# Performance work log

Hardware: AMD Instinct MI355X
Metric: run time of the kernel (lower is better)

Reference implementation:

```python
import jax, jax.numpy as jnp
import numpy as np
import math

B, W, D, H, K = 32, 512, 512, 8, 64
DH = D // H

def _rms(x, s, eps=1e-6):
    return x / jnp.sqrt(jnp.mean(x * x, axis=-1, keepdims=True) + eps) * s

def _l2n(x):
    return x / (jnp.linalg.norm(x, axis=-1, keepdims=True) + 1e-6)

def _rope(x, fc):
    b, t, h, d = x.shape
    xc = jax.lax.complex(x[..., 0::2], x[..., 1::2])
    xr = xc * fc
    return jnp.stack([xr.real, xr.imag], axis=-1).reshape(b, t, h, d)

def setup_inputs() -> dict:
    key = jax.random.key(0)
    ks = jax.random.split(key, 24)
    n = lambda i, s: jax.random.normal(ks[i], s, jnp.float32) * 0.02
    return {
        'x': jax.random.normal(ks[0], (B, W, D), jnp.float32),
        'epi_keys': _l2n(jax.random.normal(ks[1], (B, K, D), jnp.float32)),
        'epi_vals': jax.random.normal(ks[2], (B, K, D), jnp.float32),
        'epi_age': jax.random.uniform(ks[3], (B, K), jnp.float32, 0.0, 10.0),
        'epi_strength': jax.random.uniform(ks[4], (B, K), jnp.float32, 0.01, 1.0),
        'pos_idx': jnp.arange(W, dtype=jnp.int32),
        'rms1': jnp.ones((D,), jnp.float32), 'rms_kv': jnp.ones((D,), jnp.float32),
        'rms2': jnp.ones((D,), jnp.float32), 'rms_read': jnp.ones((D,), jnp.float32),
        'Wq': n(5, (D, D)), 'bq': jnp.zeros((D,), jnp.float32),
        'Wk': n(6, (D, D)), 'bk': jnp.zeros((D,), jnp.float32),
        'Wv': n(7, (D, D)), 'bv': jnp.zeros((D,), jnp.float32),
        'Wo': n(8, (D, D)), 'bo': jnp.zeros((D,), jnp.float32),
        'W1': n(9, (D, 8 * D)), 'W2': n(10, (4 * D, D)),
        'Wwk': n(11, (D, D)), 'bwk': jnp.zeros((D,), jnp.float32),
        'Wwv': n(12, (D, D)), 'bwv': jnp.zeros((D,), jnp.float32),
        'Wws': n(13, (D, 1)), 'bws': jnp.zeros((1,), jnp.float32),
        'Wg1': n(14, (D + 2, D)), 'bg1': jnp.zeros((D,), jnp.float32),
        'Wg2': n(15, (D, 1)), 'bg2': jnp.zeros((1,), jnp.float32),
    }

def _cell(x, epi_keys, epi_vals, epi_age, epi_strength, pos_idx,
          rms1, rms_kv, rms2, rms_read, Wq, bq, Wk, bk, Wv, bv, Wo, bo,
          W1, W2, Wwk, bwk, Wwv, bwv, Wws, bws, Wg1, bg1, Wg2, bg2):
    Bc, T, Dc = x.shape
    # RoPE freqs at absolute window positions (slice_freqs_cis)
    freqs = 1.0 / (10000.0 ** (jnp.arange(0, DH, 2, dtype=jnp.float32) / DH))  # (DH/2,)
    ang = pos_idx.astype(jnp.float32)[:, None] * freqs[None, :]               # (T, DH/2)
    fc = jax.lax.complex(jnp.cos(ang), jnp.sin(ang))[None, :, None, :]        # (1,T,1,DH/2)
    # --- windowed causal RoPE attention (TransformerBlock) ---
    nx, nkv = _rms(x, rms1), _rms(x, rms_kv)
    q = _rope((nx @ Wq + bq).reshape(Bc, T, H, DH), fc)
    k = _rope((nkv @ Wk + bk).reshape(Bc, T, H, DH), fc)
    v = (nkv @ Wv + bv).reshape(Bc, T, H, DH)
    att = jnp.einsum('bthd,bshd->bhts', q, k) / math.sqrt(DH)
    causal = jnp.tril(jnp.ones((T, T), bool))
    att = jnp.where(causal[None, None], att, -1e9)
    p = jax.nn.softmax(att, axis=-1)
    o = jnp.einsum('bhts,bshd->bthd', p, v).reshape(Bc, T, Dc)
    h1 = x + (o @ Wo + bo)
    gv = _rms(h1, rms2) @ W1
    g, val = jnp.split(gv, 2, axis=-1)
    h2 = h1 + (jax.nn.silu(g) * val) @ W2                                     # (B,T,D)
    # --- window summary query ---
    q_win = jnp.mean(h2, axis=1)                                              # (B,D)
    # --- EpisodicSlotReader ---
    qn = _l2n(q_win)
    kn = _l2n(epi_keys)
    sim_r = jnp.sum(kn * qn[:, None, :], axis=-1)                             # (B,K)
    logits = sim_r + 0.5 * jnp.log(jnp.clip(epi_strength, 0.001, 1e9)) - 0.02 * epi_age
    logits = logits + ((epi_strength > 0.001).astype(jnp.float32) - 1.0) * 1000.0
    w_read = jax.nn.softmax(logits, axis=-1)
    read = _rms(jnp.sum(w_read[:, :, None] * epi_vals, axis=1), rms_read)     # (B,D)
    # --- write projections ---
    write_key = q_win @ Wwk + bwk
    write_val = q_win @ Wwv + bwv
    ws = jnp.clip(jax.nn.sigmoid(q_win @ Wws + bws), 0.0, 1.0)                # (B,1)
    # --- EpisodicSlotWriter (ST top-1 competitive write) ---
    wk_n = _l2n(write_key)
    sim_w = jnp.sum(kn * wk_n[:, None, :], axis=-1)                           # (B,K)
    soft = jax.nn.softmax(sim_w * 50.0, axis=-1)
    hard = jax.nn.one_hot(jnp.argmax(soft, axis=-1), K, dtype=jnp.float32)
    write_w = jax.lax.stop_gradient(hard - soft) + soft
    eff = write_w * ws * 0.5                                                  # (B,K)
    re = eff[:, :, None]
    keys_new = _l2n((1.0 - re) * epi_keys + re * write_key[:, None, :])
    vals_new = (1.0 - re) * epi_vals + re * write_val[:, None, :]
    age_new = (epi_age + 1.0) * (1.0 - write_w)
    sn = epi_strength * 0.995
    sn = jnp.clip(sn + write_w * ws * (1.0 - sn), 0.001, 1.0)
    best_sim = jnp.max(sim_w, axis=-1)                                        # (B,)
    # --- MemoryRecallGate ---
    novelty = (1.0 - best_sim)[:, None]
    xg = jnp.concatenate([q_win, ws, novelty], axis=-1)                       # (B,D+2)
    gate = jax.nn.sigmoid(jax.nn.silu(xg @ Wg1 + bg1) @ Wg2 + bg2)            # (B,1)
    out = h2 + (gate * read)[:, None, :]
    return out, keys_new, vals_new, age_new, sn, gate

def reference(x, epi_keys, epi_vals, epi_age, epi_strength, pos_idx,
              rms1, rms_kv, rms2, rms_read, Wq, bq, Wk, bk, Wv, bv, Wo, bo,
              W1, W2, Wwk, bwk, Wwv, bwv, Wws, bws, Wg1, bg1, Wg2, bg2):
    return _cell(x, epi_keys, epi_vals, epi_age, epi_strength, pos_idx,
                 rms1, rms_kv, rms2, rms_read, Wq, bq, Wk, bk, Wv, bv, Wo, bo,
                 W1, W2, Wwk, bwk, Wwv, bwv, Wws, bws, Wg1, bg1, Wg2, bg2)
```

## Files before the change

### kernel.cpp

```cpp
#include <hip/hip_runtime.h>


#define DEVI __device__ __forceinline__
typedef unsigned short u16;
typedef unsigned int   u32;
typedef __bf16 v8bf __attribute__((ext_vector_type(8)));
typedef float  v4f  __attribute__((ext_vector_type(4)));

DEVI float bf2f(u16 u) { u32 v = ((u32)u) << 16; return __builtin_bit_cast(float, v); }
DEVI u16 f2bf(float f) {
  u32 x = __builtin_bit_cast(u32, f);
  u32 r = x + 0x7fffu + ((x >> 16) & 1u);
  return (u16)(r >> 16);
}
DEVI uint4 pack8(const float* f) {
  u32 a[4];
#pragma unroll
  for (int i = 0; i < 4; ++i)
    a[i] = (u32)f2bf(f[2*i]) | ((u32)f2bf(f[2*i+1]) << 16);
  uint4 v; v.x = a[0]; v.y = a[1]; v.z = a[2]; v.w = a[3]; return v;
}
DEVI void ld8f(const float* p, float* f) {
  float4 a = *(const float4*)p, b = *(const float4*)(p + 4);
  f[0]=a.x; f[1]=a.y; f[2]=a.z; f[3]=a.w; f[4]=b.x; f[5]=b.y; f[6]=b.z; f[7]=b.w;
}
DEVI void st8f(float* p, const float* f) {
  *(float4*)p       = make_float4(f[0], f[1], f[2], f[3]);
  *(float4*)(p + 4) = make_float4(f[4], f[5], f[6], f[7]);
}
DEVI v8bf ldfrag(const u16* p) { return __builtin_bit_cast(v8bf, *(const uint4*)p); }

DEVI void async16(const u16* g, u16* l) {
  __builtin_amdgcn_global_load_lds(
      (const __attribute__((address_space(1))) void*)g,
      (__attribute__((address_space(3))) void*)l, 16, 0, 0);
}

DEVI float wave_sum64(float v) {
  v += __shfl_xor(v, 1);  v += __shfl_xor(v, 2);  v += __shfl_xor(v, 4);
  v += __shfl_xor(v, 8);  v += __shfl_xor(v, 16); v += __shfl_xor(v, 32);
  return v;
}

__device__ float block_sum256(float v, float* sred) {
  v = wave_sum64(v);
  int w = threadIdx.x >> 6;
  __syncthreads();
  if ((threadIdx.x & 63) == 0) sred[w] = v;
  __syncthreads();
  return sred[0] + sred[1] + sred[2] + sred[3];
}

__global__ __launch_bounds__(256) void transpose_k(const float* __restrict__ in,
                                                   const float* __restrict__ scale,
                                                   u16* __restrict__ outp,
                                                   int R, int C) {
  __shared__ u16 t[32][33];
  int c0 = blockIdx.x * 32, r0 = blockIdx.y * 32;
  int lc = threadIdx.x & 31, lr = threadIdx.x >> 5;
  for (int rr = lr; rr < 32; rr += 8) {
    float v = in[(size_t)(r0 + rr) * C + c0 + lc];
    if (scale) v *= scale[r0 + rr];
    t[rr][lc] = f2bf(v);
  }
  __syncthreads();
  for (int rr = lr; rr < 32; rr += 8)
    outp[(size_t)(c0 + rr) * R + r0 + lc] = t[lc][rr];
}

__global__ __launch_bounds__(256) void rms_k(const float* __restrict__ x,
                                             u16* __restrict__ o1) {
  int w = threadIdx.x >> 6, lane = threadIdx.x & 63;
  size_t row = (size_t)blockIdx.x * 4 + w;
  float xf[8]; ld8f(x + row * 512 + lane * 8, xf);
  float ss = 0.f;
#pragma unroll
  for (int i = 0; i < 8; ++i) ss += xf[i] * xf[i];
  ss = wave_sum64(ss);
  float inv = rsqrtf(ss * (1.f / 512.f) + 1e-6f);
  float of[8];
#pragma unroll
  for (int i = 0; i < 8; ++i) of[i] = xf[i] * inv;
  *(uint4*)(o1 + row * 512 + lane * 8) = pack8(of);
}

__global__ __launch_bounds__(256) void gemm128_k(const u16* __restrict__ A,
                                                 const u16* __restrict__ BT,
                                                 const float* __restrict__ bias,
                                                 const float* __restrict__ bias2,
                                                 const float* __restrict__ resf,
                                                 u16* __restrict__ outb,
                                                 float* __restrict__ outf,
                                                 int N, int Kd) {
  __shared__ u16 As[128 * 64];
  __shared__ u16 Bs[128 * 64];
  int tid = threadIdx.x;
  int w = tid >> 6, lane = tid & 63;
  int m = lane & 15, quad = lane >> 4;
  int wm = w >> 1, wn = w & 1;
  int bm = blockIdx.x, bn = blockIdx.y;
  v4f acc[4][4] = {};
  const int gswz = ((lane & 7) ^ (lane >> 3)) * 8;
  const u16* Ag = A + (size_t)(bm * 128 + w * 32 + (lane >> 3)) * Kd + gswz;
  const u16* Bg = BT + (size_t)(bn * 128 + w * 32 + (lane >> 3)) * Kd + gswz;
  u16* Al = &As[w * 32 * 64];
  u16* Bl = &Bs[w * 32 * 64];
  const int rsw = (m & 7) * 8;
  for (int k0 = 0; k0 < Kd; k0 += 64) {
#pragma unroll
    for (int it = 0; it < 4; ++it) {
      async16(Ag + (size_t)it * 8 * Kd + k0, Al + it * 8 * 64);
      async16(Bg + (size_t)it * 8 * Kd + k0, Bl + it * 8 * 64);
    }
    __syncthreads();
#pragma unroll
    for (int kk = 0; kk < 2; ++kk) {
      v8bf af[4], bfr[4];
#pragma unroll
      for (int i = 0; i < 4; ++i)
        af[i] = ldfrag(&As[(wm * 64 + i * 16 + m) * 64 +
                           ((kk * 32 + quad * 8) ^ rsw)]);
#pragma unroll
      for (int j = 0; j < 4; ++j)
        bfr[j] = ldfrag(&Bs[(wn * 64 + j * 16 + m) * 64 +
                            ((kk * 32 + quad * 8) ^ rsw)]);
#pragma unroll
      for (int i = 0; i < 4; ++i)
#pragma unroll
        for (int j = 0; j < 4; ++j)
          acc[i][j] = __builtin_amdgcn_mfma_f32_16x16x32_bf16(af[i], bfr[j],
                                                              acc[i][j], 0, 0, 0);
    }
    __syncthreads();
  }
#pragma unroll
  for (int i = 0; i < 4; ++i) {
    int grow0 = bm * 128 + wm * 64 + i * 16 + quad * 4;
#pragma unroll
    for (int j = 0; j < 4; ++j) {
      int gcol = bn * 128 + wn * 64 + j * 16 + m;
      float bv = 0.f;
      if (bias) {
        int cc = gcol;
        const float* bp = bias;
        if (bias2 && cc >= 512) { bp = bias2; cc -= 512; }
        bv = bp[cc];
      }
#pragma unroll
      for (int rr = 0; rr < 4; ++rr) {
        size_t idx = (size_t)(grow0 + rr) * N + gcol;
        float v = acc[i][j][rr] + bv;
        if (resf) v += resf[idx];
        if (outb) outb[idx] = f2bf(v);
        else      outf[idx] = v;
      }
    }
  }
}

__global__ __launch_bounds__(256) void mlp1_k(const u16* __restrict__ A,
                                              const u16* __restrict__ W1T,
                                              u16* __restrict__ out) {
  __shared__ u16 As[128 * 64];
  __shared__ u16 Bgs[64 * 64];
  __shared__ u16 Bvs[64 * 64];
  const int Kd = 512;
  int tid = threadIdx.x;
  int w = tid >> 6, lane = tid & 63;
  int m = lane & 15, quad = lane >> 4;
  int bm = blockIdx.x, bn = blockIdx.y;
  v4f accg[2][4] = {}, accv[2][4] = {};
  const int gswz = ((lane & 7) ^ (lane >> 3)) * 8;
  const u16* Ag  = A + (size_t)(bm * 128 + w * 32 + (lane >> 3)) * Kd + gswz;
  const u16* Bgp = W1T + (size_t)(bn * 64 + w * 16 + (lane >> 3)) * Kd + gswz;
  const u16* Bvp = W1T + (size_t)(2048 + bn * 64 + w * 16 + (lane >> 3)) * Kd + gswz;
  u16* Al  = &As[w * 32 * 64];
  u16* Bgl = &Bgs[w * 16 * 64];
  u16* Bvl = &Bvs[w * 16 * 64];
  const int rsw = (m & 7) * 8;
  for (int k0 = 0; k0 < Kd; k0 += 64) {
#pragma unroll
    for (int it = 0; it < 4; ++it)
      async16(Ag + (size_t)it * 8 * Kd + k0, Al + it * 8 * 64);
#pragma unroll
    for (int it = 0; it < 2; ++it) {
      async16(Bgp + (size_t)it * 8 * Kd + k0, Bgl + it * 8 * 64);
      async16(Bvp + (size_t)it * 8 * Kd + k0, Bvl + it * 8 * 64);
    }
    __syncthreads();
#pragma unroll
    for (int kk = 0; kk < 2; ++kk) {
      v8bf af[2], bg[4], bv[4];
#pragma unroll
      for (int i = 0; i < 2; ++i)
        af[i] = ldfrag(&As[(w * 32 + i * 16 + m) * 64 +
                           ((kk * 32 + quad * 8) ^ rsw)]);
#pragma unroll
      for (int j = 0; j < 4; ++j) {
        bg[j] = ldfrag(&Bgs[(j * 16 + m) * 64 + ((kk * 32 + quad * 8) ^ rsw)]);
        bv[j] = ldfrag(&Bvs[(j * 16 + m) * 64 + ((kk * 32 + quad * 8) ^ rsw)]);
      }
#pragma unroll
      for (int i = 0; i < 2; ++i)
#pragma unroll
        for (int j = 0; j < 4; ++j) {
          accg[i][j] = __builtin_amdgcn_mfma_f32_16x16x32_bf16(af[i], bg[j],
                                                               accg[i][j], 0, 0, 0);
          accv[i][j] = __builtin_amdgcn_mfma_f32_16x16x32_bf16(af[i], bv[j],
                                                               accv[i][j], 0, 0, 0);
        }
    }
    __syncthreads();
  }
#pragma unroll
  for (int i = 0; i < 2; ++i) {
    int grow0 = bm * 128 + w * 32 + i * 16 + quad * 4;
#pragma unroll
    for (int j = 0; j < 4; ++j) {
      int gcol = bn * 64 + j * 16 + m;
#pragma unroll
      for (int rr = 0; rr < 4; ++rr) {
        float g = accg[i][j][rr];
        float sv = g / (1.f + __expf(-g));
        out[(size_t)(grow0 + rr) * 2048 + gcol] = f2bf(sv * accv[i][j][rr]);
      }
    }
  }
}

__global__ __launch_bounds__(256) void rope_k(u16* __restrict__ tnsr,
                                              const int* __restrict__ pos,
                                              int rowStride) {
  int pid = blockIdx.x * 256 + threadIdx.x;
  int f = pid & 31;
  int row = pid >> 8;
  int tt = row & 511;
  int col2 = (pid & 255) * 2;
  float freq = exp2f(-0.41524101186f * (float)f);
  float ang = (float)pos[tt] * freq;
  float sv, cv;
  sincosf(ang, &sv, &cv);
  u16* p = tnsr + (size_t)row * rowStride + col2;
  u32 v = *(u32*)p;
  float e = bf2f((u16)(v & 0xffffu)), o = bf2f((u16)(v >> 16));
  float ne = e * cv - o * sv;
  float no = e * sv + o * cv;
  *(u32*)p = (u32)f2bf(ne) | ((u32)f2bf(no) << 16);
}

__global__ __launch_bounds__(1024) void attn_k(const u16* __restrict__ qg,
                                               const u16* __restrict__ kv,
                                               u16* __restrict__ og) {
  __shared__ u16 Ks[512 * 64];
  __shared__ u16 Vt[64 * 512];
  __shared__ u16 Ps[16][16 * 40];
  int tid = threadIdx.x;
  int w = tid >> 6, lane = tid & 63;
  int m = lane & 15, quad = lane >> 4;
  int bh = blockIdx.x;
  int b = bh >> 3, h = bh & 7;
  const size_t qbase = (size_t)b * 512 * 512 + h * 64;
  const u16* kbase = kv + (size_t)b * 512 * 1024 + h * 64;
  const u16* vbase = kbase + 512;

  {
    int d8 = (tid & 7) * 8;
    for (int s = tid >> 3; s < 512; s += 128) {
      uint4 t4 = *(const uint4*)(kbase + (size_t)s * 1024 + d8);
      *(uint4*)&Ks[s * 64 + (d8 ^ ((s & 7) * 8))] = t4;
    }
  }
  {
    int d = tid & 63, sw = (d & 7) * 8;
    for (int s = tid >> 6; s < 512; s += 16)
      Vt[d * 512 + (s ^ sw)] = vbase[(size_t)s * 1024 + d];
  }
  __syncthreads();

  for (int rep = 0; rep < 2; ++rep) {
    int qt = rep == 0 ? w : 31 - w;
    int tb = qt * 16;
    const u16* qp = qg + qbase + (size_t)(tb + m) * 512;
    v8bf aq0 = ldfrag(qp + quad * 8);
    v8bf aq1 = ldfrag(qp + 32 + quad * 8);
    v4f acc[4] = {};
    float mr[4], lr_[4];
#pragma unroll
    for (int rr = 0; rr < 4; ++rr) { mr[rr] = -1.0e30f; lr_[rr] = 0.f; }
    int swz = (m & 7) * 8;

    for (int st2 = 0; st2 <= qt; st2 += 2) {
      int srA = st2 * 16 + m;
      v8bf ka0 = ldfrag(&Ks[srA * 64 + ((quad * 8) ^ swz)]);
      v8bf ka1 = ldfrag(&Ks[srA * 64 + ((32 + quad * 8) ^ swz)]);
      v4f s4a = {};
      s4a = __builtin_amdgcn_mfma_f32_16x16x32_bf16(aq0, ka0, s4a, 0, 0, 0);
      s4a = __builtin_amdgcn_mfma_f32_16x16x32_bf16(aq1, ka1, s4a, 0, 0, 0);
      bool haveB = (st2 + 1 <= qt);
      v4f s4b = {};
      if (haveB) {
        int srB = srA + 16;
        v8bf kb0 = ldfrag(&Ks[srB * 64 + ((quad * 8) ^ swz)]);
        v8bf kb1 = ldfrag(&Ks[srB * 64 + ((32 + quad * 8) ^ swz)]);
        s4b = __builtin_amdgcn_mfma_f32_16x16x32_bf16(aq0, kb0, s4b, 0, 0, 0);
        s4b = __builtin_amdgcn_mfma_f32_16x16x32_bf16(aq1, kb1, s4b, 0, 0, 0);
      }
      float sca[4], scb[4];
#pragma unroll
      for (int rr = 0; rr < 4; ++rr) {
        int rowt = tb + quad * 4 + rr;
        sca[rr] = s4a[rr] * 0.125f;
        if (st2 == qt && st2 * 16 + m > rowt) sca[rr] = -1.0e9f;
        scb[rr] = haveB ? s4b[rr] * 0.125f : -1.0e30f;
        if (haveB && st2 + 1 == qt && (st2 + 1) * 16 + m > rowt) scb[rr] = -1.0e9f;
      }
      float pva[4], pvb[4], alpha[4];
#pragma unroll
      for (int rr = 0; rr < 4; ++rr) {
        float v = fmaxf(sca[rr], scb[rr]);
        v = fmaxf(v, __shfl_xor(v, 1));
        v = fmaxf(v, __shfl_xor(v, 2));
        v = fmaxf(v, __shfl_xor(v, 4));
        v = fmaxf(v, __shfl_xor(v, 8));
        float mn = fmaxf(mr[rr], v);
        alpha[rr] = __expf(mr[rr] - mn);
        pva[rr] = __expf(sca[rr] - mn);
        pvb[rr] = __expf(scb[rr] - mn);
        mr[rr] = mn;
      }
#pragma unroll
      for (int rr = 0; rr < 4; ++rr) {
        float s = pva[rr] + pvb[rr];
        s += __shfl_xor(s, 1); s += __shfl_xor(s, 2);
        s += __shfl_xor(s, 4); s += __shfl_xor(s, 8);
        lr_[rr] = lr_[rr] * alpha[rr] + s;
#pragma unroll
        for (int c = 0; c < 4; ++c) acc[c][rr] *= alpha[rr];
        Ps[w][(quad * 4 + rr) * 40 + m]      = f2bf(pva[rr]);
        Ps[w][(quad * 4 + rr) * 40 + 16 + m] = f2bf(pvb[rr]);
      }
      __asm__ volatile("" ::: "memory");
      v8bf pf = ldfrag(&Ps[w][m * 40 + quad * 8]);
#pragma unroll
      for (int c = 0; c < 4; ++c) {
        int drow = c * 16 + m;
        v8bf vf = ldfrag(&Vt[drow * 512 +
                             ((st2 * 16 + quad * 8) ^ ((drow & 7) * 8))]);
        acc[c] = __builtin_amdgcn_mfma_f32_16x16x32_bf16(pf, vf, acc[c], 0, 0, 0);
      }
    }
#pragma unroll
    for (int rr = 0; rr < 4; ++rr) {
      int t = tb + quad * 4 + rr;
      float inv = 1.f / lr_[rr];
      u16* op = og + qbase + (size_t)t * 512;
#pragma unroll
      for (int c = 0; c < 4; ++c) op[c * 16 + m] = f2bf(acc[c][rr] * inv);
    }
  }
}

__global__ __launch_bounds__(256) void qwin_k(const float* __restrict__ h2,
                                              float* __restrict__ part) {
  int bc = blockIdx.x;
  int b = bc >> 3;
  int c = bc & 7;
  int d2 = threadIdx.x * 2;
  float a0 = 0.f, a1 = 0.f;
  for (int i = 0; i < 64; ++i) {
    int t = c * 64 + i;
    float2 v = *(const float2*)(h2 + ((size_t)(b * 512 + t)) * 512 + d2);
    a0 += v.x;
    a1 += v.y;
  }
  part[(size_t)bc * 512 + d2]     = a0;
  part[(size_t)bc * 512 + d2 + 1] = a1;
}

__global__ __launch_bounds__(256) void qw_k(const float* __restrict__ part,
                                            float* __restrict__ qw_g) {
  int b = blockIdx.x;
#pragma unroll
  for (int u = 0; u < 2; ++u) {
    int d = threadIdx.x + u * 256;
    float s = 0.f;
#pragma unroll
    for (int c = 0; c < 8; ++c) s += part[((size_t)b * 8 + c) * 512 + d];
    qw_g[(size_t)b * 512 + d] = s * (1.f / 512.f);
  }
}

__global__ __launch_bounds__(256) void gemv_k(
    const float* __restrict__ qw_g, const float* __restrict__ Wwk,
    const float* __restrict__ bwk, const float* __restrict__ Wwv,
    const float* __restrict__ bwv, const float* __restrict__ Wg1,
    const float* __restrict__ bg1, const float* __restrict__ Wws,
    const float* __restrict__ bws, float* __restrict__ wkey_g,
    float* __restrict__ wval_g, float* __restrict__ abase_g,
    float* __restrict__ ws_g) {
  __shared__ float qs[512];
  __shared__ float prt[4][64];
  __shared__ float sred[8];
  int tid = threadIdx.x;
  int b = blockIdx.y, cg = blockIdx.x;
  qs[tid]       = qw_g[(size_t)b * 512 + tid];
  qs[tid + 256] = qw_g[(size_t)b * 512 + tid + 256];
  __syncthreads();
  if (cg == 24) {
    float p = qs[tid] * Wws[tid] + qs[tid + 256] * Wws[tid + 256];
    float tot = block_sum256(p, sred);
    if (tid == 0) {
      float wsv = 1.f / (1.f + __expf(-(tot + bws[0])));
      ws_g[b] = fminf(fmaxf(wsv, 0.f), 1.f);
    }
    return;
  }
  int sel = cg >> 3;
  int c0 = (cg & 7) * 64;
  const float* W = sel == 0 ? Wwk : (sel == 1 ? Wwv : Wg1);
  const float* bias = sel == 0 ? bwk : (sel == 1 ? bwv : bg1);
  float* dst = sel == 0 ? wkey_g : (sel == 1 ? wval_g : abase_g);
  int kg = tid >> 6, cl = tid & 63;
  const float* Wp = W + (size_t)(kg * 128) * 512 + c0 + cl;
  float acc = 0.f;
#pragma unroll 8
  for (int i = 0; i < 128; ++i) acc += qs[kg * 128 + i] * Wp[(size_t)i * 512];
  prt[kg][cl] = acc;
  __syncthreads();
  if (tid < 64)
    dst[(size_t)b * 512 + c0 + tid] =
        prt[0][tid] + prt[1][tid] + prt[2][tid] + prt[3][tid] + bias[c0 + tid];
}

__global__ __launch_bounds__(256) void epi2_k(
    const float* __restrict__ qw_g, const float* __restrict__ wkey_g,
    const float* __restrict__ wval_g, const float* __restrict__ abase_g,
    const float* __restrict__ ws_g, const float* __restrict__ keys,
    const float* __restrict__ vals, const float* __restrict__ age,
    const float* __restrict__ strength, const float* __restrict__ Wg1,
    const float* __restrict__ Wg2, const float* __restrict__ bg2,
    const float* __restrict__ rms_read, float* __restrict__ read_f,
    float* __restrict__ gate_f, float* __restrict__ keys_out,
    float* __restrict__ vals_out, float* __restrict__ age_out,
    float* __restrict__ sn_out, float* __restrict__ gate_out) {
  int b = blockIdx.x;
  int tid = threadIdx.x;
  int w = tid >> 6, lane = tid & 63;
  __shared__ float qs[512], wkl[512], wvl[512];
  __shared__ float knorm[64], sr[64], swv[64], wread[64];
  __shared__ float sred[8];
  __shared__ float scal[2];
  __shared__ int bestk;
  __shared__ float novs;

  qs[tid]        = qw_g[(size_t)b * 512 + tid];
  qs[tid + 256]  = qw_g[(size_t)b * 512 + tid + 256];
  wkl[tid]       = wkey_g[(size_t)b * 512 + tid];
  wkl[tid + 256] = wkey_g[(size_t)b * 512 + tid + 256];
  wvl[tid]       = wval_g[(size_t)b * 512 + tid];
  wvl[tid + 256] = wval_g[(size_t)b * 512 + tid + 256];
  __syncthreads();
  float ws_s = ws_g[b];
  float p = qs[tid] * qs[tid] + qs[tid + 256] * qs[tid + 256];
  float tot = block_sum256(p, sred);
  if (tid == 0) scal[0] = 1.f / (sqrtf(tot) + 1e-6f);
  p = wkl[tid] * wkl[tid] + wkl[tid + 256] * wkl[tid + 256];
  tot = block_sum256(p, sred);
  if (tid == 0) scal[1] = 1.f / (sqrtf(tot) + 1e-6f);
  __syncthreads();
  float qscale = scal[0], wscale = scal[1];
  for (int k = w; k < 64; k += 4) {
    float kf[8];
    ld8f(keys + ((size_t)b * 64 + k) * 512 + lane * 8, kf);
    float s2 = 0.f, sq = 0.f, sw = 0.f;
#pragma unroll
    for (int i = 0; i < 8; ++i) {
      s2 += kf[i] * kf[i];
      sq += kf[i] * qs[lane * 8 + i];
      sw += kf[i] * wkl[lane * 8 + i];
    }
    s2 = wave_sum64(s2);
    sq = wave_sum64(sq);
    sw = wave_sum64(sw);
    if (lane == 0) {
      float kn = sqrtf(s2) + 1e-6f;
      knorm[k] = kn;
      float st = strength[b * 64 + k];
      float ag = age[b * 64 + k];
      sr[k] = (sq * qscale) / kn + 0.5f * logf(fminf(fmaxf(st, 0.001f), 1e9f)) -
              0.02f * ag + ((st > 0.001f) ? 0.f : -1000.f);
      swv[k] = (sw * wscale) / kn;
    }
  }
  __syncthreads();
  if (w == 0) {
    float v = sr[lane];
    float mx = v;
    mx = fmaxf(mx, __shfl_xor(mx, 1));  mx = fmaxf(mx, __shfl_xor(mx, 2));
    mx = fmaxf(mx, __shfl_xor(mx, 4));  mx = fmaxf(mx, __shfl_xor(mx, 8));
    mx = fmaxf(mx, __shfl_xor(mx, 16)); mx = fmaxf(mx, __shfl_xor(mx, 32));
    float e = __expf(v - mx);
    float sm = wave_sum64(e);
    wread[lane] = e / sm;
  } else if (w == 1) {
    float v = swv[lane];
    int idx = lane;
#pragma unroll
    for (int mm = 1; mm < 64; mm <<= 1) {
      float ov = __shfl_xor(v, mm);
      int oi = __shfl_xor(idx, mm);
      if (ov > v || (ov == v && oi < idx)) { v = ov; idx = oi; }
    }
    if (lane == 0) { bestk = idx; novs = 1.f - v; }
  }
  __syncthreads();
  float rv0 = 0.f, rv1 = 0.f;
  for (int k = 0; k < 64; ++k) {
    float wr = wread[k];
    const float* vp = vals + ((size_t)b * 64 + k) * 512;
    rv0 += wr * vp[tid];
    rv1 += wr * vp[tid + 256];
  }
  p = rv0 * rv0 + rv1 * rv1;
  tot = block_sum256(p, sred);
  float rinv = rsqrtf(tot * (1.f / 512.f) + 1e-6f);
  read_f[(size_t)b * 512 + tid]       = rv0 * rinv * rms_read[tid];
  read_f[(size_t)b * 512 + tid + 256] = rv1 * rinv * rms_read[tid + 256];
  if (tid < 64) {
    int k = tid;
    float hard = (k == bestk) ? 1.f : 0.f;
    float ag = age[b * 64 + k];
    age_out[b * 64 + k] = (ag + 1.f) * (1.f - hard);
    float st = strength[b * 64 + k];
    float s0 = st * 0.995f;
    float snv = s0 + hard * ws_s * (1.f - s0);
    sn_out[b * 64 + k] = fminf(fmaxf(snv, 0.001f), 1.f);
  }
  for (int k = w; k < 64; k += 4) {
    float re = (k == bestk) ? ws_s * 0.5f : 0.f;
    float kf[8], vf[8];
    ld8f(keys + ((size_t)b * 64 + k) * 512 + lane * 8, kf);
    ld8f(vals + ((size_t)b * 64 + k) * 512 + lane * 8, vf);
    float u[8], ss = 0.f;
#pragma unroll
    for (int i = 0; i < 8; ++i) {
      u[i] = (1.f - re) * kf[i] + re * wkl[lane * 8 + i];
      ss += u[i] * u[i];
    }
    ss = wave_sum64(ss);
    float uinv = 1.f / (sqrtf(ss) + 1e-6f);
    float ko[8], vo[8];
#pragma unroll
    for (int i = 0; i < 8; ++i) {
      ko[i] = u[i] * uinv;
      vo[i] = (1.f - re) * vf[i] + re * wvl[lane * 8 + i];
    }
    st8f(keys_out + ((size_t)b * 64 + k) * 512 + lane * 8, ko);
    st8f(vals_out + ((size_t)b * 64 + k) * 512 + lane * 8, vo);
  }
  __syncthreads();
  float nov = novs;
  float a0 = abase_g[(size_t)b * 512 + tid] +
             ws_s * Wg1[(size_t)512 * 512 + tid] +
             nov * Wg1[(size_t)513 * 512 + tid];
  float a1 = abase_g[(size_t)b * 512 + tid + 256] +
             ws_s * Wg1[(size_t)512 * 512 + tid + 256] +
             nov * Wg1[(size_t)513 * 512 + tid + 256];
  float h0 = a0 / (1.f + __expf(-a0));
  float h1v = a1 / (1.f + __expf(-a1));
  float gp = h0 * Wg2[tid] + h1v * Wg2[tid + 256];
  tot = block_sum256(gp, sred);
  if (tid == 0) {
    float g = 1.f / (1.f + __expf(-(tot + bg2[0])));
    gate_f[b] = g;
    gate_out[b] = g;
  }
}

__global__ __launch_bounds__(256) void final_k(const float* __restrict__ h2,
                                               const float* __restrict__ read_f,
                                               const float* __restrict__ gate_f,
                                               float* __restrict__ outp) {
  size_t i2 = ((size_t)blockIdx.x * 256 + threadIdx.x) * 2;
  int b = (int)(i2 >> 18);
  int d = (int)(i2 & 511);
  float g = gate_f[b];
  float2 h = *(const float2*)(h2 + i2);
  outp[i2]     = h.x + g * read_f[b * 512 + d];
  outp[i2 + 1] = h.y + g * read_f[b * 512 + d + 1];
}

extern "C" void kernel_launch(void* const* d_in, const int* in_sizes, int n_in,
                              void* d_out, int out_size, void* d_ws,
                              size_t ws_size, hipStream_t stream) {
  const float* x        = (const float*)d_in[0];
  const float* epi_keys = (const float*)d_in[1];
  const float* epi_vals = (const float*)d_in[2];
  const float* epi_age  = (const float*)d_in[3];
  const float* epi_str  = (const float*)d_in[4];
  const int*   pos      = (const int*)d_in[5];
  const float* rms1     = (const float*)d_in[6];
  const float* rms_kv   = (const float*)d_in[7];
  const float* rms2     = (const float*)d_in[8];
  const float* rms_read = (const float*)d_in[9];
  const float* Wq = (const float*)d_in[10]; const float* bq = (const float*)d_in[11];
  const float* Wk = (const float*)d_in[12]; const float* bk = (const float*)d_in[13];
  const float* Wv = (const float*)d_in[14]; const float* bv = (const float*)d_in[15];
  const float* Wo = (const float*)d_in[16]; const float* bo = (const float*)d_in[17];
  const float* W1 = (const float*)d_in[18]; const float* W2 = (const float*)d_in[19];
  const float* Wwk = (const float*)d_in[20]; const float* bwk = (const float*)d_in[21];
  const float* Wwv = (const float*)d_in[22]; const float* bwv = (const float*)d_in[23];
  const float* Wws = (const float*)d_in[24]; const float* bws = (const float*)d_in[25];
  const float* Wg1 = (const float*)d_in[26]; const float* bg1 = (const float*)d_in[27];
  const float* Wg2 = (const float*)d_in[28]; const float* bg2 = (const float*)d_in[29];

  float* out      = (float*)d_out;
  float* out_main = out;
  float* out_keys = out + 8388608;
  float* out_vals = out + 9437184;
  float* out_age  = out + 10485760;
  float* out_sn   = out + 10487808;
  float* out_gate = out + 10489856;

  char* w8 = (char*)d_ws;
  size_t off = 0;
  auto alloc = [&](size_t bytes) {
    char* pp = w8 + off;
    off += (bytes + 255) & ~(size_t)255;
    return pp;
  };
  u16* WTq  = (u16*)alloc(512 * 512 * 2);
  u16* WTkv = (u16*)alloc((size_t)1024 * 512 * 2);
  u16* WTo  = (u16*)alloc(512 * 512 * 2);
  u16* WT1  = (u16*)alloc((size_t)4096 * 512 * 2);
  u16* WT2  = (u16*)alloc((size_t)512 * 2048 * 2);
  const size_t TB = (size_t)16384 * 512 * 2;
  u16* nrm = (u16*)alloc(TB);
  u16* qb  = (u16*)alloc(TB);
  u16* kvb = (u16*)alloc(2 * TB);
  u16* ob  = (u16*)alloc(TB);
  u16* n2  = (u16*)alloc(TB);
  float* h1f = (float*)alloc((size_t)16384 * 512 * 4);
  u16*   gact = nrm;
  float* h2f  = (float*)ob;
  float* part    = (float*)alloc((size_t)32 * 8 * 512 * 4);
  float* qw_g    = (float*)alloc((size_t)32 * 512 * 4);
  float* wkey_g  = (float*)alloc((size_t)32 * 512 * 4);
  float* wval_g  = (float*)alloc((size_t)32 * 512 * 4);
  float* abase_g = (float*)alloc((size_t)32 * 512 * 4);
  float* ws_g    = (float*)alloc(64 * 4);
  float* read_f  = (float*)alloc((size_t)32 * 512 * 4);
  float* gate_f  = (float*)alloc(64 * 4);

  transpose_k<<<dim3(16, 16), 256, 0, stream>>>(Wq, rms1, WTq, 512, 512);
  transpose_k<<<dim3(16, 16), 256, 0, stream>>>(Wk, rms_kv, WTkv, 512, 512);
  transpose_k<<<dim3(16, 16), 256, 0, stream>>>(Wv, rms_kv, WTkv + 512 * 512, 512, 512);
  transpose_k<<<dim3(16, 16), 256, 0, stream>>>(Wo, nullptr, WTo, 512, 512);
  transpose_k<<<dim3(128, 16), 256, 0, stream>>>(W1, rms2, WT1, 512, 4096);
  transpose_k<<<dim3(16, 64), 256, 0, stream>>>(W2, nullptr, WT2, 2048, 512);
  rms_k<<<4096, 256, 0, stream>>>(x, nrm);
  gemm128_k<<<dim3(128, 4), 256, 0, stream>>>(nrm, WTq, bq, nullptr, nullptr,
                                              qb, nullptr, 512, 512);
  gemm128_k<<<dim3(128, 8), 256, 0, stream>>>(nrm, WTkv, bk, bv, nullptr,
                                              kvb, nullptr, 1024, 512);
  rope_k<<<16384, 256, 0, stream>>>(qb, pos, 512);
  rope_k<<<16384, 256, 0, stream>>>(kvb, pos, 1024);
  attn_k<<<256, 1024, 0, stream>>>(qb, kvb, ob);
  gemm128_k<<<dim3(128, 4), 256, 0, stream>>>(ob, WTo, bo, nullptr, x,
                                              nullptr, h1f, 512, 512);
  rms_k<<<4096, 256, 0, stream>>>(h1f, n2);
  mlp1_k<<<dim3(128, 32), 256, 0, stream>>>(n2, WT1, gact);
  gemm128_k<<<dim3(128, 4), 256, 0, stream>>>(gact, WT2, nullptr, nullptr, h1f,
                                              nullptr, h2f, 512, 2048);
  qwin_k<<<256, 256, 0, stream>>>(h2f, part);
  qw_k<<<32, 256, 0, stream>>>(part, qw_g);
  gemv_k<<<dim3(25, 32), 256, 0, stream>>>(qw_g, Wwk, bwk, Wwv, bwv, Wg1, bg1,
                                           Wws, bws, wkey_g, wval_g, abase_g, ws_g);
  epi2_k<<<32, 256, 0, stream>>>(qw_g, wkey_g, wval_g, abase_g, ws_g, epi_keys,
                                 epi_vals, epi_age, epi_str, Wg1, Wg2, bg2,
                                 rms_read, read_f, gate_f, out_keys, out_vals,
                                 out_age, out_sn, out_gate);
  final_k<<<16384, 256, 0, stream>>>(h2f, read_f, gate_f, out_main);
}
```

Measured before the change: 542.1 us.

## Overlap next K-tile global loads with MFMA compute in GEMM kernels

Measured after the change: 547.1 us. About the same (+0.9%).

```diff
diff --git a/kernel.cpp b/kernel.cpp
--- a/kernel.cpp
+++ b/kernel.cpp
@@ -106,31 +106,44 @@
   u16* Al = &As[w * 32 * 64];
   u16* Bl = &Bs[w * 32 * 64];
   const int rsw = (m & 7) * 8;
-  for (int k0 = 0; k0 < Kd; k0 += 64) {
-#pragma unroll
-    for (int it = 0; it < 4; ++it) {
-      async16(Ag + (size_t)it * 8 * Kd + k0, Al + it * 8 * 64);
-      async16(Bg + (size_t)it * 8 * Kd + k0, Bl + it * 8 * 64);
+  const int nt = Kd >> 6;
+#pragma unroll
+  for (int it = 0; it < 4; ++it) {
+    async16(Ag + (size_t)it * 8 * Kd, Al + it * 8 * 64);
+    async16(Bg + (size_t)it * 8 * Kd, Bl + it * 8 * 64);
+  }
+  __syncthreads();
+  for (int t = 0; t < nt; ++t) {
+    v8bf af[2][4], bfr[2][4];
+#pragma unroll
+    for (int kk = 0; kk < 2; ++kk) {
+#pragma unroll
+      for (int i = 0; i < 4; ++i)
+        af[kk][i] = ldfrag(&As[(wm * 64 + i * 16 + m) * 64 +
+                               ((kk * 32 + quad * 8) ^ rsw)]);
+#pragma unroll
+      for (int j = 0; j < 4; ++j)
+        bfr[kk][j] = ldfrag(&Bs[(wn * 64 + j * 16 + m) * 64 +
+                                ((kk * 32 + quad * 8) ^ rsw)]);
     }
     __syncthreads();
-#pragma unroll
-    for (int kk = 0; kk < 2; ++kk) {
-      v8bf af[4], bfr[4];
+    if (t + 1 < nt) {
+      int k0 = (t + 1) * 64;
+#pragma unroll
+      for (int it = 0; it < 4; ++it) {
+        async16(Ag + (size_t)it * 8 * Kd + k0, Al + it * 8 * 64);
+        async16(Bg + (size_t)it * 8 * Kd + k0, Bl + it * 8 * 64);
+      }
+    }
+#pragma unroll
+    for (int kk = 0; kk < 2; ++kk)
 #pragma unroll
       for (int i = 0; i < 4; ++i)
-        af[i] = ldfrag(&As[(wm * 64 + i * 16 + m) * 64 +
-                           ((kk * 32 + quad * 8) ^ rsw)]);
-#pragma unroll
-      for (int j = 0; j < 4; ++j)
-        bfr[j] = ldfrag(&Bs[(wn * 64 + j * 16 + m) * 64 +
-                            ((kk * 32 + quad * 8) ^ rsw)]);
-#pragma unroll
-      for (int i = 0; i < 4; ++i)
 #pragma unroll
         for (int j = 0; j < 4; ++j)
-          acc[i][j] = __builtin_amdgcn_mfma_f32_16x16x32_bf16(af[i], bfr[j],
+          acc[i][j] = __builtin_amdgcn_mfma_f32_16x16x32_bf16(af[kk][i],
+                                                              bfr[kk][j],
                                                               acc[i][j], 0, 0, 0);
-    }
     __syncthreads();
   }
 #pragma unroll
@@ -178,38 +191,55 @@
   u16* Bgl = &Bgs[w * 16 * 64];
   u16* Bvl = &Bvs[w * 16 * 64];
   const int rsw = (m & 7) * 8;
-  for (int k0 = 0; k0 < Kd; k0 += 64) {
-#pragma unroll
-    for (int it = 0; it < 4; ++it)
-      async16(Ag + (size_t)it * 8 * Kd + k0, Al + it * 8 * 64);
-#pragma unroll
-    for (int it = 0; it < 2; ++it) {
-      async16(Bgp + (size_t)it * 8 * Kd + k0, Bgl + it * 8 * 64);
-      async16(Bvp + (size_t)it * 8 * Kd + k0, Bvl + it * 8 * 64);
+  const int nt = Kd >> 6;
+#pragma unroll
+  for (int it = 0; it < 4; ++it)
+    async16(Ag + (size_t)it * 8 * Kd, Al + it * 8 * 64);
+#pragma unroll
+  for (int it = 0; it < 2; ++it) {
+    async16(Bgp + (size_t)it * 8 * Kd, Bgl + it * 8 * 64);
+    async16(Bvp + (size_t)it * 8 * Kd, Bvl + it * 8 * 64);
+  }
+  __syncthreads();
+  for (int t = 0; t < nt; ++t) {
+    v8bf af[2][2], bg[2][4], bv[2][4];
+#pragma unroll
+    for (int kk = 0; kk < 2; ++kk) {
+#pragma unroll
+      for (int i = 0; i < 2; ++i)
+        af[kk][i] = ldfrag(&As[(w * 32 + i * 16 + m) * 64 +
+                               ((kk * 32 + quad * 8) ^ rsw)]);
+#pragma unroll
+      for (int j = 0; j < 4; ++j) {
+        bg[kk][j] = ldfrag(&Bgs[(j * 16 + m) * 64 + ((kk * 32 + quad * 8) ^ rsw)]);
+        bv[kk][j] = ldfrag(&Bvs[(j * 16 + m) * 64 + ((kk * 32 + quad * 8) ^ rsw)]);
+      }
     }
     __syncthreads();
-#pragma unroll
-    for (int kk = 0; kk < 2; ++kk) {
-      v8bf af[2], bg[4], bv[4];
+    if (t + 1 < nt) {
+      int k0 = (t + 1) * 64;
+#pragma unroll
+      for (int it = 0; it < 4; ++it)
+        async16(Ag + (size_t)it * 8 * Kd + k0, Al + it * 8 * 64);
+#pragma unroll
+      for (int it = 0; it < 2; ++it) {
+        async16(Bgp + (size_t)it * 8 * Kd + k0, Bgl + it * 8 * 64);
+        async16(Bvp + (size_t)it * 8 * Kd + k0, Bvl + it * 8 * 64);
+      }
+    }
+#pragma unroll
+    for (int kk = 0; kk < 2; ++kk)
 #pragma unroll
       for (int i = 0; i < 2; ++i)
-        af[i] = ldfrag(&As[(w * 32 + i * 16 + m) * 64 +
-                           ((kk * 32 + quad * 8) ^ rsw)]);
-#pragma unroll
-      for (int j = 0; j < 4; ++j) {
-        bg[j] = ldfrag(&Bgs[(j * 16 + m) * 64 + ((kk * 32 + quad * 8) ^ rsw)]);
-        bv[j] = ldfrag(&Bvs[(j * 16 + m) * 64 + ((kk * 32 + quad * 8) ^ rsw)]);
-      }
-#pragma unroll
-      for (int i = 0; i < 2; ++i)
 #pragma unroll
         for (int j = 0; j < 4; ++j) {
-          accg[i][j] = __builtin_amdgcn_mfma_f32_16x16x32_bf16(af[i], bg[j],
+          accg[i][j] = __builtin_amdgcn_mfma_f32_16x16x32_bf16(af[kk][i],
+                                                               bg[kk][j],
                                                                accg[i][j], 0, 0, 0);
-          accv[i][j] = __builtin_amdgcn_mfma_f32_16x16x32_bf16(af[i], bv[j],
+          accv[i][j] = __builtin_amdgcn_mfma_f32_16x16x32_bf16(af[kk][i],
+                                                               bv[kk][j],
                                                                accv[i][j], 0, 0, 0);
         }
-    }
     __syncthreads();
   }
 #pragma unroll
```

## Double-buffer shared-memory tiles in GEMM and MLP1 kernels to overlap loads

Applied to the files above, without the earlier changes.

New measurement: 562.2 us. 3.7% more time.

```diff
diff --git a/kernel.cpp b/kernel.cpp
--- a/kernel.cpp
+++ b/kernel.cpp
@@ -92,8 +92,8 @@
                                                  u16* __restrict__ outb,
                                                  float* __restrict__ outf,
                                                  int N, int Kd) {
-  __shared__ u16 As[128 * 64];
-  __shared__ u16 Bs[128 * 64];
+  __shared__ u16 As[2][128 * 64];
+  __shared__ u16 Bs[2][128 * 64];
   int tid = threadIdx.x;
   int w = tid >> 6, lane = tid & 63;
   int m = lane & 15, quad = lane >> 4;
@@ -103,27 +103,29 @@
   const int gswz = ((lane & 7) ^ (lane >> 3)) * 8;
   const u16* Ag = A + (size_t)(bm * 128 + w * 32 + (lane >> 3)) * Kd + gswz;
   const u16* Bg = BT + (size_t)(bn * 128 + w * 32 + (lane >> 3)) * Kd + gswz;
-  u16* Al = &As[w * 32 * 64];
-  u16* Bl = &Bs[w * 32 * 64];
+  const int lw = w * 32 * 64;
   const int rsw = (m & 7) * 8;
-  for (int k0 = 0; k0 < Kd; k0 += 64) {
+  const int nt = Kd >> 6;
+
+  auto stage = [&](int k0, int bi) {
 #pragma unroll
     for (int it = 0; it < 4; ++it) {
-      async16(Ag + (size_t)it * 8 * Kd + k0, Al + it * 8 * 64);
-      async16(Bg + (size_t)it * 8 * Kd + k0, Bl + it * 8 * 64);
-    }
-    __syncthreads();
+      async16(Ag + (size_t)it * 8 * Kd + k0, &As[bi][lw + it * 8 * 64]);
+      async16(Bg + (size_t)it * 8 * Kd + k0, &Bs[bi][lw + it * 8 * 64]);
+    }
+  };
+  auto compute = [&](int bi) {
 #pragma unroll
     for (int kk = 0; kk < 2; ++kk) {
       v8bf af[4], bfr[4];
 #pragma unroll
       for (int i = 0; i < 4; ++i)
-        af[i] = ldfrag(&As[(wm * 64 + i * 16 + m) * 64 +
-                           ((kk * 32 + quad * 8) ^ rsw)]);
+        af[i] = ldfrag(&As[bi][(wm * 64 + i * 16 + m) * 64 +
+                               ((kk * 32 + quad * 8) ^ rsw)]);
 #pragma unroll
       for (int j = 0; j < 4; ++j)
-        bfr[j] = ldfrag(&Bs[(wn * 64 + j * 16 + m) * 64 +
-                            ((kk * 32 + quad * 8) ^ rsw)]);
+        bfr[j] = ldfrag(&Bs[bi][(wn * 64 + j * 16 + m) * 64 +
+                                ((kk * 32 + quad * 8) ^ rsw)]);
 #pragma unroll
       for (int i = 0; i < 4; ++i)
 #pragma unroll
@@ -131,6 +133,16 @@
           acc[i][j] = __builtin_amdgcn_mfma_f32_16x16x32_bf16(af[i], bfr[j],
                                                               acc[i][j], 0, 0, 0);
     }
+  };
+
+  stage(0, 0);
+  __syncthreads();
+  for (int t = 0; t < nt; t += 2) {
+    stage((t + 1) * 64, 1);
+    compute(0);
+    __syncthreads();
+    if (t + 2 < nt) stage((t + 2) * 64, 0);
+    compute(1);
     __syncthreads();
   }
 #pragma unroll
@@ -161,9 +173,9 @@
 __global__ __launch_bounds__(256) void mlp1_k(const u16* __restrict__ A,
                                               const u16* __restrict__ W1T,
                                               u16* __restrict__ out) {
-  __shared__ u16 As[128 * 64];
-  __shared__ u16 Bgs[64 * 64];
-  __shared__ u16 Bvs[64 * 64];
+  __shared__ u16 As[2][128 * 64];
+  __shared__ u16 Bgs[2][64 * 64];
+  __shared__ u16 Bvs[2][64 * 64];
   const int Kd = 512;
   int tid = threadIdx.x;
   int w = tid >> 6, lane = tid & 63;
@@ -174,31 +186,33 @@
   const u16* Ag  = A + (size_t)(bm * 128 + w * 32 + (lane >> 3)) * Kd + gswz;
   const u16* Bgp = W1T + (size_t)(bn * 64 + w * 16 + (lane >> 3)) * Kd + gswz;
   const u16* Bvp = W1T + (size_t)(2048 + bn * 64 + w * 16 + (lane >> 3)) * Kd + gswz;
-  u16* Al  = &As[w * 32 * 64];
-  u16* Bgl = &Bgs[w * 16 * 64];
-  u16* Bvl = &Bvs[w * 16 * 64];
+  const int lwA = w * 32 * 64;
+  const int lwB = w * 16 * 64;
   const int rsw = (m & 7) * 8;
-  for (int k0 = 0; k0 < Kd; k0 += 64) {
+  const int nt = Kd >> 6;
+
+  auto stage = [&](int k0, int bi) {
 #pragma unroll
     for (int it = 0; it < 4; ++it)
-      async16(Ag + (size_t)it * 8 * Kd + k0, Al + it * 8 * 64);
+      async16(Ag + (size_t)it * 8 * Kd + k0, &As[bi][lwA + it * 8 * 64]);
 #pragma unroll
     for (int it = 0; it < 2; ++it) {
-      async16(Bgp + (size_t)it * 8 * Kd + k0, Bgl + it * 8 * 64);
-      async16(Bvp + (size_t)it * 8 * Kd + k0, Bvl + it * 8 * 64);
-    }
-    __syncthreads();
+      async16(Bgp + (size_t)it * 8 * Kd + k0, &Bgs[bi][lwB + it * 8 * 64]);
+      async16(Bvp + (size_t)it * 8 * Kd + k0, &Bvs[bi][lwB + it * 8 * 64]);
+    }
+  };
+  auto compute = [&](int bi) {
 #pragma unroll
     for (int kk = 0; kk < 2; ++kk) {
       v8bf af[2], bg[4], bv[4];
 #pragma unroll
       for (int i = 0; i < 2; ++i)
-        af[i] = ldfrag(&As[(w * 32 + i * 16 + m) * 64 +
-                           ((kk * 32 + quad * 8) ^ rsw)]);
+        af[i] = ldfrag(&As[bi][(w * 32 + i * 16 + m) * 64 +
+                               ((kk * 32 + quad * 8) ^ rsw)]);
 #pragma unroll
       for (int j = 0; j < 4; ++j) {
-        bg[j] = ldfrag(&Bgs[(j * 16 + m) * 64 + ((kk * 32 + quad * 8) ^ rsw)]);
-        bv[j] = ldfrag(&Bvs[(j * 16 + m) * 64 + ((kk * 32 + quad * 8) ^ rsw)]);
+        bg[j] = ldfrag(&Bgs[bi][(j * 16 + m) * 64 + ((kk * 32 + quad * 8) ^ rsw)]);
+        bv[j] = ldfrag(&Bvs[bi][(j * 16 + m) * 64 + ((kk * 32 + quad * 8) ^ rsw)]);
       }
 #pragma unroll
       for (int i = 0; i < 2; ++i)
@@ -210,6 +224,16 @@
                                                                accv[i][j], 0, 0, 0);
         }
     }
+  };
+
+  stage(0, 0);
+  __syncthreads();
+  for (int t = 0; t < nt; t += 2) {
+    stage((t + 1) * 64, 1);
+    compute(0);
+    __syncthreads();
+    if (t + 2 < nt) stage((t + 2) * 64, 0);
+    compute(1);
     __syncthreads();
   }
 #pragma unroll
```

## Fuse QKV projection, merge weight transposes, single RoPE launch, attn MFMA priority

Applied to the files above, without the earlier changes.

New measurement: 516.4 us. 4.7% less time.

```diff
diff --git a/kernel.cpp b/kernel.cpp
--- a/kernel.cpp
+++ b/kernel.cpp
@@ -51,12 +51,30 @@
   return sred[0] + sred[1] + sred[2] + sred[3];
 }
 
-__global__ __launch_bounds__(256) void transpose_k(const float* __restrict__ in,
-                                                   const float* __restrict__ scale,
-                                                   u16* __restrict__ outp,
-                                                   int R, int C) {
+__global__ __launch_bounds__(256) void transpose_all_k(
+    const float* __restrict__ Wq, const float* __restrict__ Wk,
+    const float* __restrict__ Wv, const float* __restrict__ Wo,
+    const float* __restrict__ W1, const float* __restrict__ W2,
+    const float* __restrict__ rms1, const float* __restrict__ rms_kv,
+    const float* __restrict__ rms2, u16* __restrict__ WTqkv,
+    u16* __restrict__ WTo, u16* __restrict__ WT1, u16* __restrict__ WT2,
+    const float* __restrict__ bq, const float* __restrict__ bk,
+    const float* __restrict__ bv, float* __restrict__ bias_qkv) {
+  int id = blockIdx.x;
+  if (id >= 4096) {
+    int j = (id - 4096) * 256 + threadIdx.x;
+    bias_qkv[j] = j < 512 ? bq[j] : (j < 1024 ? bk[j - 512] : bv[j - 1024]);
+    return;
+  }
+  const float* in; const float* scale; u16* outp; int R, C, bx, by;
+  if (id < 256)       { in=Wq; scale=rms1;   outp=WTqkv;            R=512;  C=512;  int l=id;       bx=l&15;  by=l>>4; }
+  else if (id < 512)  { in=Wk; scale=rms_kv; outp=WTqkv+512*512;    R=512;  C=512;  int l=id-256;   bx=l&15;  by=l>>4; }
+  else if (id < 768)  { in=Wv; scale=rms_kv; outp=WTqkv+1024*512;   R=512;  C=512;  int l=id-512;   bx=l&15;  by=l>>4; }
+  else if (id < 1024) { in=Wo; scale=nullptr;outp=WTo;              R=512;  C=512;  int l=id-768;   bx=l&15;  by=l>>4; }
+  else if (id < 3072) { in=W1; scale=rms2;   outp=WT1;              R=512;  C=4096; int l=id-1024;  bx=l&127; by=l>>7; }
+  else                { in=W2; scale=nullptr;outp=WT2;              R=2048; C=512;  int l=id-3072;  bx=l&15;  by=l>>4; }
   __shared__ u16 t[32][33];
-  int c0 = blockIdx.x * 32, r0 = blockIdx.y * 32;
+  int c0 = bx * 32, r0 = by * 32;
   int lc = threadIdx.x & 31, lr = threadIdx.x >> 5;
   for (int rr = lr; rr < 32; rr += 8) {
     float v = in[(size_t)(r0 + rr) * C + c0 + lc];
@@ -87,7 +105,6 @@
 __global__ __launch_bounds__(256) void gemm128_k(const u16* __restrict__ A,
                                                  const u16* __restrict__ BT,
                                                  const float* __restrict__ bias,
-                                                 const float* __restrict__ bias2,
                                                  const float* __restrict__ resf,
                                                  u16* __restrict__ outb,
                                                  float* __restrict__ outf,
@@ -139,13 +156,7 @@
 #pragma unroll
     for (int j = 0; j < 4; ++j) {
       int gcol = bn * 128 + wn * 64 + j * 16 + m;
-      float bv = 0.f;
-      if (bias) {
-        int cc = gcol;
-        const float* bp = bias;
-        if (bias2 && cc >= 512) { bp = bias2; cc -= 512; }
-        bv = bp[cc];
-      }
+      float bv = bias ? bias[gcol] : 0.f;
 #pragma unroll
       for (int rr = 0; rr < 4; ++rr) {
         size_t idx = (size_t)(grow0 + rr) * N + gcol;
@@ -228,19 +239,21 @@
   }
 }
 
-__global__ __launch_bounds__(256) void rope_k(u16* __restrict__ tnsr,
-                                              const int* __restrict__ pos,
-                                              int rowStride) {
+__global__ __launch_bounds__(256) void rope_qk_k(u16* __restrict__ qkv,
+                                                 const int* __restrict__ pos) {
   int pid = blockIdx.x * 256 + threadIdx.x;
-  int f = pid & 31;
-  int row = pid >> 8;
+  int half = pid >> 22;
+  int sub = pid & 0x3FFFFF;
+  int row = sub >> 8;
+  int pr = sub & 255;
   int tt = row & 511;
-  int col2 = (pid & 255) * 2;
+  int col2 = half * 512 + pr * 2;
+  int f = pr & 31;
   float freq = exp2f(-0.41524101186f * (float)f);
   float ang = (float)pos[tt] * freq;
   float sv, cv;
   sincosf(ang, &sv, &cv);
-  u16* p = tnsr + (size_t)row * rowStride + col2;
+  u16* p = qkv + (size_t)row * 1536 + col2;
   u32 v = *(u32*)p;
   float e = bf2f((u16)(v & 0xffffu)), o = bf2f((u16)(v >> 16));
   float ne = e * cv - o * sv;
@@ -248,8 +261,7 @@
   *(u32*)p = (u32)f2bf(ne) | ((u32)f2bf(no) << 16);
 }
 
-__global__ __launch_bounds__(1024) void attn_k(const u16* __restrict__ qg,
-                                               const u16* __restrict__ kv,
+__global__ __launch_bounds__(1024) void attn_k(const u16* __restrict__ qkv,
                                                u16* __restrict__ og) {
   __shared__ u16 Ks[512 * 64];
   __shared__ u16 Vt[64 * 512];
@@ -259,28 +271,29 @@
   int m = lane & 15, quad = lane >> 4;
   int bh = blockIdx.x;
   int b = bh >> 3, h = bh & 7;
-  const size_t qbase = (size_t)b * 512 * 512 + h * 64;
-  const u16* kbase = kv + (size_t)b * 512 * 1024 + h * 64;
+  const size_t qbase = (size_t)b * 512 * 1536 + h * 64;
+  const size_t obase = (size_t)b * 512 * 512 + h * 64;
+  const u16* kbase = qkv + (size_t)b * 512 * 1536 + 512 + h * 64;
   const u16* vbase = kbase + 512;
 
   {
     int d8 = (tid & 7) * 8;
     for (int s = tid >> 3; s < 512; s += 128) {
-      uint4 t4 = *(const uint4*)(kbase + (size_t)s * 1024 + d8);
+      uint4 t4 = *(const uint4*)(kbase + (size_t)s * 1536 + d8);
       *(uint4*)&Ks[s * 64 + (d8 ^ ((s & 7) * 8))] = t4;
     }
   }
   {
     int d = tid & 63, sw = (d & 7) * 8;
     for (int s = tid >> 6; s < 512; s += 16)
-      Vt[d * 512 + (s ^ sw)] = vbase[(size_t)s * 1024 + d];
+      Vt[d * 512 + (s ^ sw)] = vbase[(size_t)s * 1536 + d];
   }
   __syncthreads();
 
   for (int rep = 0; rep < 2; ++rep) {
     int qt = rep == 0 ? w : 31 - w;
     int tb = qt * 16;
-    const u16* qp = qg + qbase + (size_t)(tb + m) * 512;
+    const u16* qp = qkv + qbase + (size_t)(tb + m) * 1536;
     v8bf aq0 = ldfrag(qp + quad * 8);
     v8bf aq1 = ldfrag(qp + 32 + quad * 8);
     v4f acc[4] = {};
@@ -294,16 +307,20 @@
       v8bf ka0 = ldfrag(&Ks[srA * 64 + ((quad * 8) ^ swz)]);
       v8bf ka1 = ldfrag(&Ks[srA * 64 + ((32 + quad * 8) ^ swz)]);
       v4f s4a = {};
+      __builtin_amdgcn_s_setprio(1);
       s4a = __builtin_amdgcn_mfma_f32_16x16x32_bf16(aq0, ka0, s4a, 0, 0, 0);
       s4a = __builtin_amdgcn_mfma_f32_16x16x32_bf16(aq1, ka1, s4a, 0, 0, 0);
+      __builtin_amdgcn_s_setprio(0);
       bool haveB = (st2 + 1 <= qt);
       v4f s4b = {};
       if (haveB) {
         int srB = srA + 16;
         v8bf kb0 = ldfrag(&Ks[srB * 64 + ((quad * 8) ^ swz)]);
         v8bf kb1 = ldfrag(&Ks[srB * 64 + ((32 + quad * 8) ^ swz)]);
+        __builtin_amdgcn_s_setprio(1);
         s4b = __builtin_amdgcn_mfma_f32_16x16x32_bf16(aq0, kb0, s4b, 0, 0, 0);
         s4b = __builtin_amdgcn_mfma_f32_16x16x32_bf16(aq1, kb1, s4b, 0, 0, 0);
+        __builtin_amdgcn_s_setprio(0);
       }
       float sca[4], scb[4];
 #pragma unroll
@@ -341,6 +358,7 @@
       }
       __asm__ volatile("" ::: "memory");
       v8bf pf = ldfrag(&Ps[w][m * 40 + quad * 8]);
+      __builtin_amdgcn_s_setprio(1);
 #pragma unroll
       for (int c = 0; c < 4; ++c) {
         int drow = c * 16 + m;
@@ -348,12 +366,13 @@
                              ((st2 * 16 + quad * 8) ^ ((drow & 7) * 8))]);
         acc[c] = __builtin_amdgcn_mfma_f32_16x16x32_bf16(pf, vf, acc[c], 0, 0, 0);
       }
+      __builtin_amdgcn_s_setprio(0);
     }
 #pragma unroll
     for (int rr = 0; rr < 4; ++rr) {
       int t = tb + quad * 4 + rr;
       float inv = 1.f / lr_[rr];
-      u16* op = og + qbase + (size_t)t * 512;
+      u16* op = og + obase + (size_t)t * 512;
 #pragma unroll
       for (int c = 0; c < 4; ++c) op[c * 16 + m] = f2bf(acc[c][rr] * inv);
     }
@@ -629,20 +648,19 @@
     off += (bytes + 255) & ~(size_t)255;
     return pp;
   };
-  u16* WTq  = (u16*)alloc(512 * 512 * 2);
-  u16* WTkv = (u16*)alloc((size_t)1024 * 512 * 2);
-  u16* WTo  = (u16*)alloc(512 * 512 * 2);
-  u16* WT1  = (u16*)alloc((size_t)4096 * 512 * 2);
-  u16* WT2  = (u16*)alloc((size_t)512 * 2048 * 2);
+  u16* WTqkv = (u16*)alloc((size_t)1536 * 512 * 2);
+  u16* WTo   = (u16*)alloc(512 * 512 * 2);
+  u16* WT1   = (u16*)alloc((size_t)4096 * 512 * 2);
+  u16* WT2   = (u16*)alloc((size_t)512 * 2048 * 2);
   const size_t TB = (size_t)16384 * 512 * 2;
-  u16* nrm = (u16*)alloc(TB);
-  u16* qb  = (u16*)alloc(TB);
-  u16* kvb = (u16*)alloc(2 * TB);
-  u16* ob  = (u16*)alloc(TB);
-  u16* n2  = (u16*)alloc(TB);
+  u16* nrm  = (u16*)alloc(TB);
+  u16* qkvb = (u16*)alloc(3 * TB);
+  u16* ob   = (u16*)alloc(TB);
+  u16* n2   = (u16*)alloc(TB);
   float* h1f = (float*)alloc((size_t)16384 * 512 * 4);
   u16*   gact = nrm;
   float* h2f  = (float*)ob;
+  float* bias_qkv = (float*)alloc(1536 * 4);
   float* part    = (float*)alloc((size_t)32 * 8 * 512 * 4);
   float* qw_g    = (float*)alloc((size_t)32 * 512 * 4);
   float* wkey_g  = (float*)alloc((size_t)32 * 512 * 4);
@@ -652,25 +670,19 @@
   float* read_f  = (float*)alloc((size_t)32 * 512 * 4);
   float* gate_f  = (float*)alloc(64 * 4);
 
-  transpose_k<<<dim3(16, 16), 256, 0, stream>>>(Wq, rms1, WTq, 512, 512);
-  transpose_k<<<dim3(16, 16), 256, 0, stream>>>(Wk, rms_kv, WTkv, 512, 512);
-  transpose_k<<<dim3(16, 16), 256, 0, stream>>>(Wv, rms_kv, WTkv + 512 * 512, 512, 512);
-  transpose_k<<<dim3(16, 16), 256, 0, stream>>>(Wo, nullptr, WTo, 512, 512);
-  transpose_k<<<dim3(128, 16), 256, 0, stream>>>(W1, rms2, WT1, 512, 4096);
-  transpose_k<<<dim3(16, 64), 256, 0, stream>>>(W2, nullptr, WT2, 2048, 512);
+  transpose_all_k<<<4102, 256, 0, stream>>>(Wq, Wk, Wv, Wo, W1, W2, rms1,
+                                            rms_kv, rms2, WTqkv, WTo, WT1,
+                                            WT2, bq, bk, bv, bias_qkv);
   rms_k<<<4096, 256, 0, stream>>>(x, nrm);
-  gemm128_k<<<dim3(128, 4), 256, 0, stream>>>(nrm, WTq, bq, nullptr, nullptr,
-                                              qb, nullptr, 512, 512);
-  gemm128_k<<<dim3(128, 8), 256, 0, stream>>>(nrm, WTkv, bk, bv, nullptr,
-                                              kvb, nullptr, 1024, 512);
-  rope_k<<<16384, 256, 0, stream>>>(qb, pos, 512);
-  rope_k<<<16384, 256, 0, stream>>>(kvb, pos, 1024);
-  attn_k<<<256, 1024, 0, stream>>>(qb, kvb, ob);
-  gemm128_k<<<dim3(128, 4), 256, 0, stream>>>(ob, WTo, bo, nullptr, x,
+  gemm128_k<<<dim3(128, 12), 256, 0, stream>>>(nrm, WTqkv, bias_qkv, nullptr,
+                                               qkvb, nullptr, 1536, 512);
+  rope_qk_k<<<32768, 256, 0, stream>>>(qkvb, pos);
+  attn_k<<<256, 1024, 0, stream>>>(qkvb, ob);
+  gemm128_k<<<dim3(128, 4), 256, 0, stream>>>(ob, WTo, bo, x,
                                               nullptr, h1f, 512, 512);
   rms_k<<<4096, 256, 0, stream>>>(h1f, n2);
   mlp1_k<<<dim3(128, 32), 256, 0, stream>>>(n2, WT1, gact);
-  gemm128_k<<<dim3(128, 4), 256, 0, stream>>>(gact, WT2, nullptr, nullptr, h1f,
+  gemm128_k<<<dim3(128, 4), 256, 0, stream>>>(gact, WT2, nullptr, h1f,
                                               nullptr, h2f, 512, 2048);
   qwin_k<<<256, 256, 0, stream>>>(h2f, part);
   qw_k<<<32, 256, 0, stream>>>(part, qw_g);
```
